# Optimization experiments

Hardware: AMD Instinct MI355X
Metric: run time of the kernel (lower is better)

The kernel has to match this reference:

```python
import jax, jax.numpy as jnp
import numpy as np

N_HID, N_HEAD, N_K, N_V = 1024, 16, 64, 64
B, S = 2, 2048


def setup_inputs() -> dict:
    key = jax.random.key(0)
    ks = jax.random.split(key, 5)
    w_scale = 1.0 / np.sqrt(N_HID)  # keep pre-softmax logits in a sane range
    x = jax.random.normal(ks[0], (B, S, N_HID), dtype=jnp.float32)
    mask = jax.random.randint(ks[1], (B, S, N_HEAD, S), 0, 2) > 0  # [B, Sq, H, Sk] bool
    W_qkv = jax.random.normal(ks[2], (N_HID, N_HEAD * (2 * N_K + N_V)), dtype=jnp.float32) * w_scale
    b_qkv = jnp.zeros((N_HEAD * (2 * N_K + N_V),), dtype=jnp.float32)
    W_out = jax.random.normal(ks[3], (N_HEAD * N_V, N_HID), dtype=jnp.float32) * w_scale
    b_out = jnp.zeros((N_HID,), dtype=jnp.float32)
    return {"x": x, "mask": mask, "W_qkv": W_qkv, "b_qkv": b_qkv, "W_out": W_out, "b_out": b_out}


def reference(x, mask, W_qkv, b_qkv, W_out, b_out):
    nb, sl, nh = x.shape
    qkv = x @ W_qkv + b_qkv                                  # [B, S, H*(2k+v)]
    qkv = qkv.reshape(nb, sl, N_HEAD, 2 * N_K + N_V).transpose(0, 2, 1, 3)  # [B, H, S, 2k+v]
    q, k, v = qkv[..., :N_K], qkv[..., N_K:2 * N_K], qkv[..., 2 * N_K:]
    qk = jnp.einsum('bhqd,bhkd->bhqk', q, k) / np.sqrt(N_K)  # [B, H, Sq, Sk]
    # original masks on the [B, Sq, H, Sk] view; swap mask axes instead of qk
    mask_bhqk = jnp.swapaxes(mask, 1, 2)                     # [B, H, Sq, Sk]
    qk = jnp.where(mask_bhqk, qk, -jnp.inf)
    attn = jax.nn.softmax(qk, axis=-1)
    ctx = jnp.einsum('bhqk,bhkd->bhqd', attn, v)             # [B, H, S, n_v]
    ctx = ctx.transpose(0, 2, 1, 3).reshape(nb, sl, N_HEAD * N_V)
    out = ctx @ W_out + b_out
    return x + out
```

## Files before the change

### kernel.cpp

```cpp
#include <hip/hip_runtime.h>

#define SEQ 2048
#define NHEAD 16
#define NHID 1024

typedef __attribute__((ext_vector_type(8))) short bf16x8;
typedef __attribute__((ext_vector_type(4))) float f32x4;
typedef unsigned short u16;

__device__ inline u16 f2bf(float f) {
    union { float f; unsigned u; } v; v.f = f;
    unsigned r = v.u + 0x7FFFu + ((v.u >> 16) & 1u);
    return (u16)(r >> 16);
}

typedef __attribute__((address_space(3))) unsigned int  lds_uint;
typedef const __attribute__((address_space(1))) unsigned int glob_uint;
__device__ __forceinline__ void gl2lds16(const void* g, void* l) {
    __builtin_amdgcn_global_load_lds((glob_uint*)(unsigned long long)g,
                                     (lds_uint*)(unsigned int)(unsigned long long)l,
                                     16, 0, 0);
}

__global__ void cast_kernel(const float* __restrict__ in, u16* __restrict__ out, int n4) {
    int i = blockIdx.x * 256 + threadIdx.x;
    if (i < n4) {
        float4 v = ((const float4*)in)[i];
        ushort4 o;
        o.x = f2bf(v.x); o.y = f2bf(v.y); o.z = f2bf(v.z); o.w = f2bf(v.w);
        ((ushort4*)out)[i] = o;
    }
}

__global__ void transpose_cast(const float* __restrict__ in, u16* __restrict__ out, int R, int C) {
    __shared__ float tile[32][33];
    int bx = blockIdx.x * 32, by = blockIdx.y * 32;
    int tx = threadIdx.x & 31, ty = threadIdx.x >> 5;
#pragma unroll
    for (int i = ty; i < 32; i += 8) tile[i][tx] = in[(size_t)(by + i) * C + bx + tx];
    __syncthreads();
#pragma unroll
    for (int i = ty; i < 32; i += 8) out[(size_t)(bx + i) * R + by + tx] = f2bf(tile[tx][i]);
}

__global__ void transpose_v(const u16* __restrict__ in, u16* __restrict__ out) {
    __shared__ u16 tile[32][33];
    int s0 = blockIdx.x * 32, d0 = blockIdx.y * 32, bh = blockIdx.z;
    int tx = threadIdx.x & 31, ty = threadIdx.x >> 5;
    const u16* ip = in + (size_t)bh * SEQ * 64;
    u16* op = out + (size_t)bh * 64 * SEQ;
#pragma unroll
    for (int i = ty; i < 32; i += 8) tile[i][tx] = ip[(size_t)(s0 + i) * 64 + d0 + tx];
    __syncthreads();
#pragma unroll
    for (int i = ty; i < 32; i += 8) op[(size_t)(d0 + i) * SEQ + s0 + tx] = tile[tx][i];
}

__launch_bounds__(256, 2)
__global__ void gemm_qkv(const u16* __restrict__ A, const u16* __restrict__ Bt,
                         const float* __restrict__ bias,
                         u16* __restrict__ qs, u16* __restrict__ ks, u16* __restrict__ vs) {
    __shared__ __align__(16) u16 Alds[128 * 64];
    __shared__ __align__(16) u16 Blds[128 * 64];
    const int tid = threadIdx.x;
    const int m0 = blockIdx.y * 128, n0 = blockIdx.x * 128;
    const int lane = tid & 63, wid = tid >> 6;
    const int wm = (wid & 1) * 64, wn = (wid >> 1) * 64;
    const int col = lane & 15, quad = lane >> 4;
    const int sr = tid >> 3, scg = (tid & 7) * 8;
    f32x4 acc[4][4] = {};
    for (int k0 = 0; k0 < 1024; k0 += 64) {
#pragma unroll
        for (int p = 0; p < 4; p++) {
            int r = sr + p * 32;
            gl2lds16(&A[(size_t)(m0 + r) * 1024 + k0 + scg], &Alds[(p * 32 + wid * 8) * 64]);
            gl2lds16(&Bt[(size_t)(n0 + r) * 1024 + k0 + scg], &Blds[(p * 32 + wid * 8) * 64]);
        }
        __syncthreads();
#pragma unroll
        for (int kc = 0; kc < 2; kc++) {
            bf16x8 af[4], bfr[4];
#pragma unroll
            for (int t = 0; t < 4; t++) {
                af[t]  = *(const bf16x8*)&Alds[(wm + t * 16 + col) * 64 + kc * 32 + quad * 8];
                bfr[t] = *(const bf16x8*)&Blds[(wn + t * 16 + col) * 64 + kc * 32 + quad * 8];
            }
#pragma unroll
            for (int mt = 0; mt < 4; mt++)
#pragma unroll
                for (int nt = 0; nt < 4; nt++)
                    acc[mt][nt] = __builtin_amdgcn_mfma_f32_16x16x32_bf16(af[mt], bfr[nt], acc[mt][nt], 0, 0, 0);
        }
        __syncthreads();
    }
#pragma unroll
    for (int mt = 0; mt < 4; mt++)
#pragma unroll
        for (int nt = 0; nt < 4; nt++)
#pragma unroll
            for (int r = 0; r < 4; r++) {
                int gm = m0 + wm + mt * 16 + quad * 4 + r;
                int gn = n0 + wn + nt * 16 + col;
                float val = acc[mt][nt][r] + bias[gn];
                int b = gm >> 11, s = gm & 2047;
                int h = gn / 192, rr = gn - h * 192;
                size_t base = ((size_t)(b * NHEAD + h) * SEQ + s) * 64;
                if (rr < 64)       qs[base + rr] = f2bf(val * 0.125f);
                else if (rr < 128) ks[base + rr - 64] = f2bf(val);
                else               vs[base + rr - 128] = f2bf(val);
            }
}

#define MFIX 10.0f
__launch_bounds__(256, 3)
__global__ void attn_kernel(const u16* __restrict__ qs, const u16* __restrict__ ks,
                            const u16* __restrict__ vt, const int* __restrict__ mask,
                            u16* __restrict__ ctx) {
    __shared__ __align__(16) u16 Klds[2][64 * 64];
    __shared__ __align__(16) u16 Vlds[2][64 * 64];
    __shared__ __align__(16) u16 Pst[4][16 * 72];
    const int tid = threadIdx.x;
    const int lane = tid & 63, wid = tid >> 6;
    const int col = lane & 15, quad = lane >> 4;
    const int bh = blockIdx.y, b = bh >> 4, h = bh & 15;
    const int q0 = blockIdx.x * 64 + wid * 16;
    const size_t hbase = (size_t)bh * SEQ * 64;

    const int srow = lane >> 3, scol8 = (lane & 7) * 8;

    const u16* qp = qs + hbase + (size_t)(q0 + col) * 64 + quad * 8;
    bf16x8 aq0 = *(const bf16x8*)qp;
    bf16x8 aq1 = *(const bf16x8*)(qp + 32);

    const int* mp = mask + (((size_t)b * SEQ + (q0 + col)) * NHEAD + h) * SEQ + quad * 4;

    float l_lane = 0.f;
    f32x4 O[4] = {};

#pragma unroll
    for (int p = 0; p < 2; p++) {
        int rw = wid * 16 + p * 8;
        gl2lds16(&ks[hbase + (size_t)(rw + srow) * 64 + scol8], &Klds[0][rw * 64]);
        gl2lds16(&vt[((size_t)bh * 64 + rw + srow) * SEQ + scol8], &Vlds[0][rw * 64]);
    }

    for (int it = 0; it < 32; it++) {
        const int cur = it & 1;
        const int kb = it * 64;
        __syncthreads();
        if (it < 31) {
#pragma unroll
            for (int p = 0; p < 2; p++) {
                int rw = wid * 16 + p * 8;
                gl2lds16(&ks[hbase + (size_t)(kb + 64 + rw + srow) * 64 + scol8], &Klds[cur ^ 1][rw * 64]);
                gl2lds16(&vt[((size_t)bh * 64 + rw + srow) * SEQ + kb + 64 + scol8], &Vlds[cur ^ 1][rw * 64]);
            }
        }
        int4 mv[4];
#pragma unroll
        for (int nt = 0; nt < 4; nt++) mv[nt] = *(const int4*)(mp + kb + nt * 16);

        f32x4 st[4];
#pragma unroll
        for (int nt = 0; nt < 4; nt++) {
            bf16x8 ka0 = *(const bf16x8*)&Klds[cur][(nt * 16 + col) * 64 + quad * 8];
            bf16x8 ka1 = *(const bf16x8*)&Klds[cur][(nt * 16 + col) * 64 + 32 + quad * 8];
            f32x4 z = {};
            z = __builtin_amdgcn_mfma_f32_16x16x32_bf16(ka0, aq0, z, 0, 0, 0);
            z = __builtin_amdgcn_mfma_f32_16x16x32_bf16(ka1, aq1, z, 0, 0, 0);
            st[nt] = z;
        }
#pragma unroll
        for (int nt = 0; nt < 4; nt++) {
            const int* mw = &mv[nt].x;
            float p0 = mw[0] ? __expf(st[nt][0] - MFIX) : 0.f;
            float p1 = mw[1] ? __expf(st[nt][1] - MFIX) : 0.f;
            float p2 = mw[2] ? __expf(st[nt][2] - MFIX) : 0.f;
            float p3 = mw[3] ? __expf(st[nt][3] - MFIX) : 0.f;
            l_lane += (p0 + p1) + (p2 + p3);
            ushort4 pw;
            pw.x = f2bf(p0); pw.y = f2bf(p1); pw.z = f2bf(p2); pw.w = f2bf(p3);
            *(ushort4*)&Pst[wid][col * 72 + nt * 16 + quad * 4] = pw;
        }

        bf16x8 bp0 = *(const bf16x8*)&Pst[wid][col * 72 + quad * 8];
        bf16x8 bp1 = *(const bf16x8*)&Pst[wid][col * 72 + 32 + quad * 8];
#pragma unroll
        for (int dt = 0; dt < 4; dt++) {
            bf16x8 va0 = *(const bf16x8*)&Vlds[cur][(dt * 16 + col) * 64 + quad * 8];
            bf16x8 va1 = *(const bf16x8*)&Vlds[cur][(dt * 16 + col) * 64 + 32 + quad * 8];
            O[dt] = __builtin_amdgcn_mfma_f32_16x16x32_bf16(va0, bp0, O[dt], 0, 0, 0);
            O[dt] = __builtin_amdgcn_mfma_f32_16x16x32_bf16(va1, bp1, O[dt], 0, 0, 0);
        }
    }
    l_lane += __shfl_xor(l_lane, 16);
    l_lane += __shfl_xor(l_lane, 32);
    float rinv = 1.f / l_lane;
    const int q = q0 + col;
#pragma unroll
    for (int dt = 0; dt < 4; dt++) {
        ushort4 o;
        o.x = f2bf(O[dt][0] * rinv);
        o.y = f2bf(O[dt][1] * rinv);
        o.z = f2bf(O[dt][2] * rinv);
        o.w = f2bf(O[dt][3] * rinv);
        *(ushort4*)&ctx[(size_t)(b * SEQ + q) * NHID + h * 64 + dt * 16 + quad * 4] = o;
    }
}

__launch_bounds__(256, 2)
__global__ void gemm_out(const u16* __restrict__ A, const u16* __restrict__ Bt,
                         const float* __restrict__ bias, const float* __restrict__ xres,
                         float* __restrict__ out) {
    __shared__ __align__(16) u16 Alds[128 * 64];
    __shared__ __align__(16) u16 Blds[128 * 64];
    const int tid = threadIdx.x;
    const int m0 = blockIdx.y * 128, n0 = blockIdx.x * 128;
    const int lane = tid & 63, wid = tid >> 6;
    const int wm = (wid & 1) * 64, wn = (wid >> 1) * 64;
    const int col = lane & 15, quad = lane >> 4;
    const int sr = tid >> 3, scg = (tid & 7) * 8;
    f32x4 acc[4][4] = {};
    for (int k0 = 0; k0 < 1024; k0 += 64) {
#pragma unroll
        for (int p = 0; p < 4; p++) {
            int r = sr + p * 32;
            gl2lds16(&A[(size_t)(m0 + r) * 1024 + k0 + scg], &Alds[(p * 32 + wid * 8) * 64]);
            gl2lds16(&Bt[(size_t)(n0 + r) * 1024 + k0 + scg], &Blds[(p * 32 + wid * 8) * 64]);
        }
        __syncthreads();
#pragma unroll
        for (int kc = 0; kc < 2; kc++) {
            bf16x8 af[4], bfr[4];
#pragma unroll
            for (int t = 0; t < 4; t++) {
                af[t]  = *(const bf16x8*)&Alds[(wm + t * 16 + col) * 64 + kc * 32 + quad * 8];
                bfr[t] = *(const bf16x8*)&Blds[(wn + t * 16 + col) * 64 + kc * 32 + quad * 8];
            }
#pragma unroll
            for (int mt = 0; mt < 4; mt++)
#pragma unroll
                for (int nt = 0; nt < 4; nt++)
                    acc[mt][nt] = __builtin_amdgcn_mfma_f32_16x16x32_bf16(af[mt], bfr[nt], acc[mt][nt], 0, 0, 0);
        }
        __syncthreads();
    }
#pragma unroll
    for (int mt = 0; mt < 4; mt++)
#pragma unroll
        for (int nt = 0; nt < 4; nt++)
#pragma unroll
            for (int r = 0; r < 4; r++) {
                int gm = m0 + wm + mt * 16 + quad * 4 + r;
                int gn = n0 + wn + nt * 16 + col;
                out[(size_t)gm * NHID + gn] = acc[mt][nt][r] + bias[gn] + xres[(size_t)gm * NHID + gn];
            }
}

extern "C" void kernel_launch(void* const* d_in, const int* in_sizes, int n_in,
                              void* d_out, int out_size, void* d_ws, size_t ws_size,
                              hipStream_t stream) {
    const float* x     = (const float*)d_in[0];
    const int*   mask  = (const int*)d_in[1];
    const float* W_qkv = (const float*)d_in[2];
    const float* b_qkv = (const float*)d_in[3];
    const float* W_out = (const float*)d_in[4];
    const float* b_out = (const float*)d_in[5];
    float* out = (float*)d_out;

    char* ws = (char*)d_ws;
    u16* x_bf   = (u16*)(ws);
    u16* wqkv_t = (u16*)(ws + (size_t)(8  << 20));
    u16* wout_t = (u16*)(ws + (size_t)(14 << 20));
    u16* qs     = (u16*)(ws + (size_t)(16 << 20));
    u16* ks     = (u16*)(ws + (size_t)(24 << 20));
    u16* vs     = (u16*)(ws + (size_t)(32 << 20));
    u16* vt     = (u16*)(ws + (size_t)(40 << 20));
    u16* ctx    = (u16*)(ws + (size_t)(48 << 20));

    cast_kernel<<<4096, 256, 0, stream>>>(x, x_bf, 4096 * 1024 / 4);
    transpose_cast<<<dim3(3072 / 32, 1024 / 32), 256, 0, stream>>>(W_qkv, wqkv_t, 1024, 3072);
    transpose_cast<<<dim3(1024 / 32, 1024 / 32), 256, 0, stream>>>(W_out, wout_t, 1024, 1024);
    gemm_qkv<<<dim3(24, 32), 256, 0, stream>>>(x_bf, wqkv_t, b_qkv, qs, ks, vs);
    transpose_v<<<dim3(SEQ / 32, 2, 32), 256, 0, stream>>>(vs, vt);
    attn_kernel<<<dim3(32, 32), 256, 0, stream>>>(qs, ks, vt, mask, ctx);
    gemm_out<<<dim3(8, 32), 256, 0, stream>>>(ctx, wout_t, b_out, x, out);
}
```

Measured before the change: 842.8 us.

## Pack attention mask into bitmasks inside QKV GEMM epilogue

```diff
diff --git a/kernel.cpp b/kernel.cpp
--- a/kernel.cpp
+++ b/kernel.cpp
@@ -7,6 +7,7 @@
 typedef __attribute__((ext_vector_type(8))) short bf16x8;
 typedef __attribute__((ext_vector_type(4))) float f32x4;
 typedef unsigned short u16;
+typedef unsigned long long u64;
 
 __device__ inline u16 f2bf(float f) {
     union { float f; unsigned u; } v; v.f = f;
@@ -59,7 +60,8 @@
 __launch_bounds__(256, 2)
 __global__ void gemm_qkv(const u16* __restrict__ A, const u16* __restrict__ Bt,
                          const float* __restrict__ bias,
-                         u16* __restrict__ qs, u16* __restrict__ ks, u16* __restrict__ vs) {
+                         u16* __restrict__ qs, u16* __restrict__ ks, u16* __restrict__ vs,
+                         const int* __restrict__ mask, u64* __restrict__ packed) {
     __shared__ __align__(16) u16 Alds[128 * 64];
     __shared__ __align__(16) u16 Blds[128 * 64];
     const int tid = threadIdx.x;
@@ -109,12 +111,36 @@
                 else if (rr < 128) ks[base + rr - 64] = f2bf(val);
                 else               vs[base + rr - 128] = f2bf(val);
             }
+
+    const int NCHUNK = 2 * SEQ * NHEAD * (SEQ / 64);
+    const int bid = blockIdx.y * gridDim.x + blockIdx.x;
+    const int w = bid * 4 + wid;
+    for (int c0 = w * 8; c0 < NCHUNK; c0 += 3072 * 8) {
+        int vv[8];
+#pragma unroll
+        for (int u = 0; u < 8; u++) {
+            int c = c0 + u;
+            int kb = c & 31, t = c >> 5;
+            int h = t & 15, q = (t >> 4) & 2047, b = t >> 15;
+            vv[u] = mask[(((size_t)(b * SEQ + q) * NHEAD + h) * SEQ) + kb * 64 + lane];
+        }
+#pragma unroll
+        for (int u = 0; u < 8; u++) {
+            u64 bal = __ballot(vv[u] != 0);
+            if (lane == 0) {
+                int c = c0 + u;
+                int kb = c & 31, t = c >> 5;
+                int h = t & 15, q = (t >> 4) & 2047, b = t >> 15;
+                packed[((size_t)((b * NHEAD + h) * SEQ + q)) * 32 + kb] = bal;
+            }
+        }
+    }
 }
 
 #define MFIX 10.0f
 __launch_bounds__(256, 3)
 __global__ void attn_kernel(const u16* __restrict__ qs, const u16* __restrict__ ks,
-                            const u16* __restrict__ vt, const int* __restrict__ mask,
+                            const u16* __restrict__ vt, const u64* __restrict__ packed,
                             u16* __restrict__ ctx) {
     __shared__ __align__(16) u16 Klds[2][64 * 64];
     __shared__ __align__(16) u16 Vlds[2][64 * 64];
@@ -132,7 +158,8 @@
     bf16x8 aq0 = *(const bf16x8*)qp;
     bf16x8 aq1 = *(const bf16x8*)(qp + 32);
 
-    const int* mp = mask + (((size_t)b * SEQ + (q0 + col)) * NHEAD + h) * SEQ + quad * 4;
+    const u64* mpk = packed + ((size_t)bh * SEQ + (q0 + col)) * 32;
+    const int shbase = quad * 4;
 
     float l_lane = 0.f;
     f32x4 O[4] = {};
@@ -143,11 +170,13 @@
         gl2lds16(&ks[hbase + (size_t)(rw + srow) * 64 + scol8], &Klds[0][rw * 64]);
         gl2lds16(&vt[((size_t)bh * 64 + rw + srow) * SEQ + scol8], &Vlds[0][rw * 64]);
     }
+    u64 mcur = mpk[0];
 
     for (int it = 0; it < 32; it++) {
         const int cur = it & 1;
         const int kb = it * 64;
         __syncthreads();
+        u64 mnext = 0;
         if (it < 31) {
 #pragma unroll
             for (int p = 0; p < 2; p++) {
@@ -155,10 +184,8 @@
                 gl2lds16(&ks[hbase + (size_t)(kb + 64 + rw + srow) * 64 + scol8], &Klds[cur ^ 1][rw * 64]);
                 gl2lds16(&vt[((size_t)bh * 64 + rw + srow) * SEQ + kb + 64 + scol8], &Vlds[cur ^ 1][rw * 64]);
             }
-        }
-        int4 mv[4];
-#pragma unroll
-        for (int nt = 0; nt < 4; nt++) mv[nt] = *(const int4*)(mp + kb + nt * 16);
+            mnext = mpk[it + 1];
+        }
 
         f32x4 st[4];
 #pragma unroll
@@ -172,16 +199,17 @@
         }
 #pragma unroll
         for (int nt = 0; nt < 4; nt++) {
-            const int* mw = &mv[nt].x;
-            float p0 = mw[0] ? __expf(st[nt][0] - MFIX) : 0.f;
-            float p1 = mw[1] ? __expf(st[nt][1] - MFIX) : 0.f;
-            float p2 = mw[2] ? __expf(st[nt][2] - MFIX) : 0.f;
-            float p3 = mw[3] ? __expf(st[nt][3] - MFIX) : 0.f;
+            unsigned bits = (unsigned)(mcur >> (nt * 16 + shbase));
+            float p0 = (bits & 1u) ? __expf(st[nt][0] - MFIX) : 0.f;
+            float p1 = (bits & 2u) ? __expf(st[nt][1] - MFIX) : 0.f;
+            float p2 = (bits & 4u) ? __expf(st[nt][2] - MFIX) : 0.f;
+            float p3 = (bits & 8u) ? __expf(st[nt][3] - MFIX) : 0.f;
             l_lane += (p0 + p1) + (p2 + p3);
             ushort4 pw;
             pw.x = f2bf(p0); pw.y = f2bf(p1); pw.z = f2bf(p2); pw.w = f2bf(p3);
             *(ushort4*)&Pst[wid][col * 72 + nt * 16 + quad * 4] = pw;
         }
+        mcur = mnext;
 
         bf16x8 bp0 = *(const bf16x8*)&Pst[wid][col * 72 + quad * 8];
         bf16x8 bp1 = *(const bf16x8*)&Pst[wid][col * 72 + 32 + quad * 8];
@@ -277,12 +305,13 @@
     u16* vs     = (u16*)(ws + (size_t)(32 << 20));
     u16* vt     = (u16*)(ws + (size_t)(40 << 20));
     u16* ctx    = (u16*)(ws + (size_t)(48 << 20));
+    u64* packed = (u64*)(ws + (size_t)(56 << 20));
 
     cast_kernel<<<4096, 256, 0, stream>>>(x, x_bf, 4096 * 1024 / 4);
     transpose_cast<<<dim3(3072 / 32, 1024 / 32), 256, 0, stream>>>(W_qkv, wqkv_t, 1024, 3072);
     transpose_cast<<<dim3(1024 / 32, 1024 / 32), 256, 0, stream>>>(W_out, wout_t, 1024, 1024);
-    gemm_qkv<<<dim3(24, 32), 256, 0, stream>>>(x_bf, wqkv_t, b_qkv, qs, ks, vs);
+    gemm_qkv<<<dim3(24, 32), 256, 0, stream>>>(x_bf, wqkv_t, b_qkv, qs, ks, vs, mask, packed);
     transpose_v<<<dim3(SEQ / 32, 2, 32), 256, 0, stream>>>(vs, vt);
-    attn_kernel<<<dim3(32, 32), 256, 0, stream>>>(qs, ks, vt, mask, ctx);
+    attn_kernel<<<dim3(32, 32), 256, 0, stream>>>(qs, ks, vt, packed, ctx);
     gemm_out<<<dim3(8, 32), 256, 0, stream>>>(ctx, wout_t, b_out, x, out);
 }
```

New measurement: 906.1 us. 1.08x slower.

## Pad K/V LDS tiles and stage loads through registers

Applied to the files above, without the earlier changes.

```diff
diff --git a/kernel.cpp b/kernel.cpp
--- a/kernel.cpp
+++ b/kernel.cpp
@@ -112,13 +112,14 @@
 }
 
 #define MFIX 10.0f
+#define KP 72
 __launch_bounds__(256, 3)
 __global__ void attn_kernel(const u16* __restrict__ qs, const u16* __restrict__ ks,
                             const u16* __restrict__ vt, const int* __restrict__ mask,
                             u16* __restrict__ ctx) {
-    __shared__ __align__(16) u16 Klds[2][64 * 64];
-    __shared__ __align__(16) u16 Vlds[2][64 * 64];
-    __shared__ __align__(16) u16 Pst[4][16 * 72];
+    __shared__ __align__(16) u16 Klds[2][64 * KP];
+    __shared__ __align__(16) u16 Vlds[2][64 * KP];
+    __shared__ __align__(16) u16 Pst[4][16 * KP];
     const int tid = threadIdx.x;
     const int lane = tid & 63, wid = tid >> 6;
     const int col = lane & 15, quad = lane >> 4;
@@ -126,7 +127,7 @@
     const int q0 = blockIdx.x * 64 + wid * 16;
     const size_t hbase = (size_t)bh * SEQ * 64;
 
-    const int srow = lane >> 3, scol8 = (lane & 7) * 8;
+    const int srow = tid >> 3, schk = (tid & 7) * 8;
 
     const u16* qp = qs + hbase + (size_t)(q0 + col) * 64 + quad * 8;
     bf16x8 aq0 = *(const bf16x8*)qp;
@@ -137,24 +138,28 @@
     float l_lane = 0.f;
     f32x4 O[4] = {};
 
-#pragma unroll
-    for (int p = 0; p < 2; p++) {
-        int rw = wid * 16 + p * 8;
-        gl2lds16(&ks[hbase + (size_t)(rw + srow) * 64 + scol8], &Klds[0][rw * 64]);
-        gl2lds16(&vt[((size_t)bh * 64 + rw + srow) * SEQ + scol8], &Vlds[0][rw * 64]);
-    }
+    {
+        bf16x8 k0 = *(const bf16x8*)&ks[hbase + (size_t)srow * 64 + schk];
+        bf16x8 k1 = *(const bf16x8*)&ks[hbase + (size_t)(srow + 32) * 64 + schk];
+        bf16x8 v0 = *(const bf16x8*)&vt[((size_t)bh * 64 + srow) * SEQ + schk];
+        bf16x8 v1 = *(const bf16x8*)&vt[((size_t)bh * 64 + srow + 32) * SEQ + schk];
+        *(bf16x8*)&Klds[0][srow * KP + schk] = k0;
+        *(bf16x8*)&Klds[0][(srow + 32) * KP + schk] = k1;
+        *(bf16x8*)&Vlds[0][srow * KP + schk] = v0;
+        *(bf16x8*)&Vlds[0][(srow + 32) * KP + schk] = v1;
+    }
+    __syncthreads();
 
     for (int it = 0; it < 32; it++) {
         const int cur = it & 1;
         const int kb = it * 64;
-        __syncthreads();
+
+        bf16x8 nk0, nk1, nv0, nv1;
         if (it < 31) {
-#pragma unroll
-            for (int p = 0; p < 2; p++) {
-                int rw = wid * 16 + p * 8;
-                gl2lds16(&ks[hbase + (size_t)(kb + 64 + rw + srow) * 64 + scol8], &Klds[cur ^ 1][rw * 64]);
-                gl2lds16(&vt[((size_t)bh * 64 + rw + srow) * SEQ + kb + 64 + scol8], &Vlds[cur ^ 1][rw * 64]);
-            }
+            nk0 = *(const bf16x8*)&ks[hbase + (size_t)(kb + 64 + srow) * 64 + schk];
+            nk1 = *(const bf16x8*)&ks[hbase + (size_t)(kb + 64 + srow + 32) * 64 + schk];
+            nv0 = *(const bf16x8*)&vt[((size_t)bh * 64 + srow) * SEQ + kb + 64 + schk];
+            nv1 = *(const bf16x8*)&vt[((size_t)bh * 64 + srow + 32) * SEQ + kb + 64 + schk];
         }
         int4 mv[4];
 #pragma unroll
@@ -163,8 +168,8 @@
         f32x4 st[4];
 #pragma unroll
         for (int nt = 0; nt < 4; nt++) {
-            bf16x8 ka0 = *(const bf16x8*)&Klds[cur][(nt * 16 + col) * 64 + quad * 8];
-            bf16x8 ka1 = *(const bf16x8*)&Klds[cur][(nt * 16 + col) * 64 + 32 + quad * 8];
+            bf16x8 ka0 = *(const bf16x8*)&Klds[cur][(nt * 16 + col) * KP + quad * 8];
+            bf16x8 ka1 = *(const bf16x8*)&Klds[cur][(nt * 16 + col) * KP + 32 + quad * 8];
             f32x4 z = {};
             z = __builtin_amdgcn_mfma_f32_16x16x32_bf16(ka0, aq0, z, 0, 0, 0);
             z = __builtin_amdgcn_mfma_f32_16x16x32_bf16(ka1, aq1, z, 0, 0, 0);
@@ -180,17 +185,25 @@
             l_lane += (p0 + p1) + (p2 + p3);
             ushort4 pw;
             pw.x = f2bf(p0); pw.y = f2bf(p1); pw.z = f2bf(p2); pw.w = f2bf(p3);
-            *(ushort4*)&Pst[wid][col * 72 + nt * 16 + quad * 4] = pw;
-        }
-
-        bf16x8 bp0 = *(const bf16x8*)&Pst[wid][col * 72 + quad * 8];
-        bf16x8 bp1 = *(const bf16x8*)&Pst[wid][col * 72 + 32 + quad * 8];
+            *(ushort4*)&Pst[wid][col * KP + nt * 16 + quad * 4] = pw;
+        }
+
+        bf16x8 bp0 = *(const bf16x8*)&Pst[wid][col * KP + quad * 8];
+        bf16x8 bp1 = *(const bf16x8*)&Pst[wid][col * KP + 32 + quad * 8];
 #pragma unroll
         for (int dt = 0; dt < 4; dt++) {
-            bf16x8 va0 = *(const bf16x8*)&Vlds[cur][(dt * 16 + col) * 64 + quad * 8];
-            bf16x8 va1 = *(const bf16x8*)&Vlds[cur][(dt * 16 + col) * 64 + 32 + quad * 8];
+            bf16x8 va0 = *(const bf16x8*)&Vlds[cur][(dt * 16 + col) * KP + quad * 8];
+            bf16x8 va1 = *(const bf16x8*)&Vlds[cur][(dt * 16 + col) * KP + 32 + quad * 8];
             O[dt] = __builtin_amdgcn_mfma_f32_16x16x32_bf16(va0, bp0, O[dt], 0, 0, 0);
             O[dt] = __builtin_amdgcn_mfma_f32_16x16x32_bf16(va1, bp1, O[dt], 0, 0, 0);
+        }
+
+        if (it < 31) {
+            *(bf16x8*)&Klds[cur ^ 1][srow * KP + schk] = nk0;
+            *(bf16x8*)&Klds[cur ^ 1][(srow + 32) * KP + schk] = nk1;
+            *(bf16x8*)&Vlds[cur ^ 1][srow * KP + schk] = nv0;
+            *(bf16x8*)&Vlds[cur ^ 1][(srow + 32) * KP + schk] = nv1;
+            __syncthreads();
         }
     }
     l_lane += __shfl_xor(l_lane, 16);
```

Result: no change. 840.8 us (-0.2%).
